# Optimization experiments

Measured on AMD Instinct MI355X. Metric: run time of the kernel, lower is better.

Reference implementation:

```python
import jax, jax.numpy as jnp
import numpy as np

B, N, D = 128, 131072, 1

def setup_inputs() -> dict:
    key = jax.random.key(0)
    k1, k2, k3, k4, k5 = jax.random.split(key, 5)
    particles = jax.random.normal(k1, (B, N, D), dtype=jnp.float32)
    particle_weights = jax.random.uniform(k2, (B, N), dtype=jnp.float32)
    observation = jax.random.normal(k3, (B, 1), dtype=jnp.float32)
    noise = jax.random.normal(k4, (B, N, D), dtype=jnp.float32)  # std-normal; scaled by sqrt(10) inside
    uniforms = jax.random.uniform(k5, (B, N), dtype=jnp.float32)
    return {
        "particles": particles,
        "particle_weights": particle_weights,
        "observation": observation,
        "noise": noise,
        "uniforms": uniforms,
        "timestep_number": 3,
    }

def _resample(particles, particle_weights, uniforms):
    # Efficient equivalent of the original O(B*N^2) tile + argmax(cumsum >= u):
    # first index where cumsum >= u  ==  searchsorted(cumsum, u, side='left').
    cum = jnp.cumsum(particle_weights, axis=-1)            # [B, N]
    idx = jax.vmap(lambda c, u: jnp.searchsorted(c, u, side='left'))(cum, uniforms)  # [B, N]
    resampled = jnp.take_along_axis(particles, idx[..., None], axis=1)  # [B, N, D]
    n = particles.shape[1]
    resampled_w = jnp.full(particle_weights.shape, 1.0 / n, dtype=particle_weights.dtype)
    return resampled, resampled_w

def reference(particles, particle_weights, observation, noise, uniforms, timestep_number):
    # Note: the original forward calls resample_particles but then builds the
    # transition from the ORIGINAL particles; resampled values never reach the
    # outputs. We keep the call for fidelity (XLA will DCE it).
    _resampled, _rw = _resample(particles, particle_weights, uniforms)

    # UNGM transition: x/2 + 25*x/(x^2+1) + 8*cos(1.2*t) + N(0, 10)
    mean = particles / 2.0 + 25.0 * (particles / (particles ** 2 + 1.0))
    mean = mean + 8.0 * jnp.cos(1.2 * jnp.float32(timestep_number))
    new_particles = mean + noise * np.float32(np.sqrt(10.0))   # [B, N, 1]

    # Observation likelihood: y ~ N(x^2/20, 1)
    obs_mean = (new_particles ** 2 / 20.0)[..., 0]             # [B, N]
    log_prob = -0.5 * (observation - obs_mean) ** 2 - 0.5 * np.float32(np.log(2.0 * np.pi))
    w = particle_weights * jnp.exp(log_prob)                   # [B, N]
    w = w / jnp.sum(w, axis=1, keepdims=True)
    return new_particles, w
```

## Files before the change

### kernel.cpp

```cpp
#include <hip/hip_runtime.h>
#include <math.h>

#define PF_B 128
#define PF_N 131072
#define TPB 256
#define EPT 8
#define EPB (TPB * EPT)
#define BLOCKS_PER_BATCH (PF_N / EPB)


__global__ __launch_bounds__(TPB) void pf_compute(
    const float* __restrict__ particles,
    const float* __restrict__ weights,
    const float* __restrict__ obs,
    const float* __restrict__ noise,
    const int*   __restrict__ tstep,
    float* __restrict__ np_out,
    float* __restrict__ w_out,
    float* __restrict__ sums)
{
    const int b     = blockIdx.x / BLOCKS_PER_BATCH;
    const int chunk = blockIdx.x % BLOCKS_PER_BATCH;
    const long base = (long)b * PF_N + (long)chunk * EPB;

    const float ob  = obs[b];
    const float c   = 8.0f * cosf(1.2f * (float)(*tstep));
    const float sq10 = 3.16227770f;
    const float nhl2pi = -0.9189385f;

    float lsum = 0.0f;

    #pragma unroll
    for (int k = 0; k < EPT / 4; ++k) {
        const long idx = base + (long)k * (TPB * 4) + (long)threadIdx.x * 4;
        const float4 x4  = *(const float4*)(particles + idx);
        const float4 n4  = *(const float4*)(noise + idx);
        const float4 wt4 = *(const float4*)(weights + idx);

        float xs[4] = {x4.x, x4.y, x4.z, x4.w};
        float ns[4] = {n4.x, n4.y, n4.z, n4.w};
        float ws[4] = {wt4.x, wt4.y, wt4.z, wt4.w};
        float xn[4], wn[4];

        #pragma unroll
        for (int j = 0; j < 4; ++j) {
            const float x = xs[j];
            const float mean = x * 0.5f + 25.0f * (x / (x * x + 1.0f)) + c;
            const float xnew = mean + ns[j] * sq10;
            xn[j] = xnew;
            const float om = (xnew * xnew) / 20.0f;
            const float d  = ob - om;
            const float lp = -0.5f * d * d + nhl2pi;
            const float wv = ws[j] * expf(lp);
            wn[j] = wv;
            lsum += wv;
        }

        float4 o4; o4.x = xn[0]; o4.y = xn[1]; o4.z = xn[2]; o4.w = xn[3];
        float4 w4; w4.x = wn[0]; w4.y = wn[1]; w4.z = wn[2]; w4.w = wn[3];
        *(float4*)(np_out + idx) = o4;
        *(float4*)(w_out + idx)  = w4;
    }

    #pragma unroll
    for (int off = 32; off > 0; off >>= 1)
        lsum += __shfl_down(lsum, off, 64);

    __shared__ float red[TPB / 64];
    if ((threadIdx.x & 63) == 0) red[threadIdx.x >> 6] = lsum;
    __syncthreads();
    if (threadIdx.x == 0) {
        float s = 0.0f;
        #pragma unroll
        for (int i = 0; i < TPB / 64; ++i) s += red[i];
        atomicAdd(&sums[b], s);
    }
}

__global__ __launch_bounds__(TPB) void pf_normalize(
    float* __restrict__ w_out,
    const float* __restrict__ sums)
{
    const int b     = blockIdx.x / BLOCKS_PER_BATCH;
    const int chunk = blockIdx.x % BLOCKS_PER_BATCH;
    const long base = (long)b * PF_N + (long)chunk * EPB;
    const float inv = 1.0f / sums[b];

    #pragma unroll
    for (int k = 0; k < EPT / 4; ++k) {
        const long idx = base + (long)k * (TPB * 4) + (long)threadIdx.x * 4;
        float4 v = *(const float4*)(w_out + idx);
        v.x *= inv; v.y *= inv; v.z *= inv; v.w *= inv;
        *(float4*)(w_out + idx) = v;
    }
}

extern "C" void kernel_launch(void* const* d_in, const int* in_sizes, int n_in,
                              void* d_out, int out_size, void* d_ws, size_t ws_size,
                              hipStream_t stream) {
    const float* particles = (const float*)d_in[0];
    const float* weights   = (const float*)d_in[1];
    const float* obs       = (const float*)d_in[2];
    const float* noise     = (const float*)d_in[3];
    const int*   tstep     = (const int*)d_in[5];

    float* np_out = (float*)d_out;
    float* w_out  = (float*)d_out + (long)PF_B * PF_N;
    float* sums   = (float*)d_ws;

    hipMemsetAsync(d_ws, 0, PF_B * sizeof(float), stream);

    const int grid = PF_B * BLOCKS_PER_BATCH;
    pf_compute<<<grid, TPB, 0, stream>>>(particles, weights, obs, noise, tstep,
                                         np_out, w_out, sums);
    pf_normalize<<<grid, TPB, 0, stream>>>(w_out, sums);
}
```

Baseline: 337.5 us.

## Fuse compute and normalize via cooperative grid sync with weights held in registers

Measured after the change: 391.6 us. 1.16x slower.

```diff
diff --git a/kernel.cpp b/kernel.cpp
--- a/kernel.cpp
+++ b/kernel.cpp
@@ -1,15 +1,74 @@
 #include <hip/hip_runtime.h>
+#include <hip/hip_cooperative_groups.h>
 #include <math.h>
 
 #define PF_B 128
 #define PF_N 131072
 #define TPB 256
-#define EPT 8
-#define EPB (TPB * EPT)
-#define BLOCKS_PER_BATCH (PF_N / EPB)
-
-
-__global__ __launch_bounds__(TPB) void pf_compute(
+
+#define C_NBLK 512
+#define C_BPB (C_NBLK / PF_B)
+#define C_EPB (PF_N / C_BPB)
+#define C_ITERS (C_EPB / (TPB * 4))
+
+#define F_EPT 8
+#define F_EPB (TPB * F_EPT)
+#define F_BPB (PF_N / F_EPB)
+#define F_GRID (PF_B * F_BPB)
+
+namespace cg = cooperative_groups;
+
+typedef float nfloat4 __attribute__((ext_vector_type(4)));
+
+__device__ __forceinline__ void nt_store4(float* p, float4 v) {
+    nfloat4 nv; nv.x = v.x; nv.y = v.y; nv.z = v.z; nv.w = v.w;
+    __builtin_nontemporal_store(nv, (nfloat4*)p);
+}
+
+__device__ __forceinline__ void compute4(const float4 x4, const float4 n4,
+                                         const float4 wt4, float ob, float c,
+                                         float4* xn_out, float4* wv_out,
+                                         float* lsum) {
+    const float sq10   = 3.16227770f;
+    const float nhl2pi = -0.9189385f;
+    float xs[4] = {x4.x, x4.y, x4.z, x4.w};
+    float ns[4] = {n4.x, n4.y, n4.z, n4.w};
+    float ws[4] = {wt4.x, wt4.y, wt4.z, wt4.w};
+    float xn[4], wn[4];
+    #pragma unroll
+    for (int j = 0; j < 4; ++j) {
+        const float x    = xs[j];
+        const float mean = x * 0.5f
+                         + 25.0f * x * __builtin_amdgcn_rcpf(x * x + 1.0f)
+                         + c;
+        const float xnew = mean + ns[j] * sq10;
+        xn[j] = xnew;
+        const float om = (xnew * xnew) * 0.05f;
+        const float d  = ob - om;
+        const float wv = ws[j] * __expf(-0.5f * d * d + nhl2pi);
+        wn[j] = wv;
+        *lsum += wv;
+    }
+    xn_out->x = xn[0]; xn_out->y = xn[1]; xn_out->z = xn[2]; xn_out->w = xn[3];
+    wv_out->x = wn[0]; wv_out->y = wn[1]; wv_out->z = wn[2]; wv_out->w = wn[3];
+}
+
+__device__ __forceinline__ void block_reduce_atomic(float lsum, float* target,
+                                                    float* red) {
+    #pragma unroll
+    for (int off = 32; off > 0; off >>= 1)
+        lsum += __shfl_down(lsum, off, 64);
+    if ((threadIdx.x & 63) == 0) red[threadIdx.x >> 6] = lsum;
+    __syncthreads();
+    if (threadIdx.x == 0) {
+        float s = 0.0f;
+        #pragma unroll
+        for (int i = 0; i < TPB / 64; ++i) s += red[i];
+        atomicAdd(target, s);
+    }
+}
+
+__global__ __launch_bounds__(TPB, 2) void pf_fused(
     const float* __restrict__ particles,
     const float* __restrict__ weights,
     const float* __restrict__ obs,
@@ -19,79 +78,111 @@
     float* __restrict__ w_out,
     float* __restrict__ sums)
 {
-    const int b     = blockIdx.x / BLOCKS_PER_BATCH;
-    const int chunk = blockIdx.x % BLOCKS_PER_BATCH;
-    const long base = (long)b * PF_N + (long)chunk * EPB;
-
-    const float ob  = obs[b];
-    const float c   = 8.0f * cosf(1.2f * (float)(*tstep));
-    const float sq10 = 3.16227770f;
-    const float nhl2pi = -0.9189385f;
+    const int b     = blockIdx.x / C_BPB;
+    const int chunk = blockIdx.x % C_BPB;
+    const long base = (long)b * PF_N + (long)chunk * C_EPB;
+
+    const float ob = obs[b];
+    const float c  = 8.0f * cosf(1.2f * (float)(*tstep));
+
+    float4 wreg[C_ITERS];
+    float  lsum = 0.0f;
+
+    #pragma unroll
+    for (int i = 0; i < C_ITERS; ++i) {
+        const long idx = base + (long)i * (TPB * 4) + (long)threadIdx.x * 4;
+        const float4 x4  = *(const float4*)(particles + idx);
+        const float4 n4  = *(const float4*)(noise + idx);
+        const float4 wt4 = *(const float4*)(weights + idx);
+        float4 xn, wv;
+        compute4(x4, n4, wt4, ob, c, &xn, &wv, &lsum);
+        nt_store4(np_out + idx, xn);
+        wreg[i] = wv;
+    }
+
+    __shared__ float red[TPB / 64];
+    __shared__ float s_inv;
+    block_reduce_atomic(lsum, &sums[b], red);
+
+    cg::this_grid().sync();
+
+    if (threadIdx.x == 0)
+        s_inv = 1.0f / atomicAdd(&sums[b], 0.0f);
+    __syncthreads();
+    const float inv = s_inv;
+
+    #pragma unroll
+    for (int i = 0; i < C_ITERS; ++i) {
+        const long idx = base + (long)i * (TPB * 4) + (long)threadIdx.x * 4;
+        float4 w4 = wreg[i];
+        w4.x *= inv; w4.y *= inv; w4.z *= inv; w4.w *= inv;
+        nt_store4(w_out + idx, w4);
+    }
+}
+
+__global__ __launch_bounds__(TPB) void pf_pass1(
+    const float* __restrict__ particles,
+    const float* __restrict__ weights,
+    const float* __restrict__ obs,
+    const float* __restrict__ noise,
+    const int*   __restrict__ tstep,
+    float* __restrict__ np_out,
+    float* __restrict__ sums)
+{
+    const int b     = blockIdx.x / F_BPB;
+    const int chunk = blockIdx.x % F_BPB;
+    const long base = (long)b * PF_N + (long)chunk * F_EPB;
+
+    const float ob = obs[b];
+    const float c  = 8.0f * cosf(1.2f * (float)(*tstep));
 
     float lsum = 0.0f;
-
-    #pragma unroll
-    for (int k = 0; k < EPT / 4; ++k) {
+    #pragma unroll
+    for (int k = 0; k < F_EPT / 4; ++k) {
         const long idx = base + (long)k * (TPB * 4) + (long)threadIdx.x * 4;
         const float4 x4  = *(const float4*)(particles + idx);
         const float4 n4  = *(const float4*)(noise + idx);
         const float4 wt4 = *(const float4*)(weights + idx);
-
+        float4 xn, wv;
+        compute4(x4, n4, wt4, ob, c, &xn, &wv, &lsum);
+        *(float4*)(np_out + idx) = xn;
+    }
+
+    __shared__ float red[TPB / 64];
+    block_reduce_atomic(lsum, &sums[b], red);
+}
+
+__global__ __launch_bounds__(TPB) void pf_pass2(
+    const float* __restrict__ np_out,
+    const float* __restrict__ weights,
+    const float* __restrict__ obs,
+    const float* __restrict__ sums,
+    float* __restrict__ w_out)
+{
+    const int b     = blockIdx.x / F_BPB;
+    const int chunk = blockIdx.x % F_BPB;
+    const long base = (long)b * PF_N + (long)chunk * F_EPB;
+
+    const float ob     = obs[b];
+    const float inv    = 1.0f / sums[b];
+    const float nhl2pi = -0.9189385f;
+
+    #pragma unroll
+    for (int k = 0; k < F_EPT / 4; ++k) {
+        const long idx = base + (long)k * (TPB * 4) + (long)threadIdx.x * 4;
+        const float4 x4  = *(const float4*)(np_out + idx);
+        const float4 wt4 = *(const float4*)(weights + idx);
         float xs[4] = {x4.x, x4.y, x4.z, x4.w};
-        float ns[4] = {n4.x, n4.y, n4.z, n4.w};
         float ws[4] = {wt4.x, wt4.y, wt4.z, wt4.w};
-        float xn[4], wn[4];
-
+        float wn[4];
         #pragma unroll
         for (int j = 0; j < 4; ++j) {
-            const float x = xs[j];
-            const float mean = x * 0.5f + 25.0f * (x / (x * x + 1.0f)) + c;
-            const float xnew = mean + ns[j] * sq10;
-            xn[j] = xnew;
-            const float om = (xnew * xnew) / 20.0f;
+            const float om = (xs[j] * xs[j]) * 0.05f;
             const float d  = ob - om;
-            const float lp = -0.5f * d * d + nhl2pi;
-            const float wv = ws[j] * expf(lp);
-            wn[j] = wv;
-            lsum += wv;
+            wn[j] = ws[j] * __expf(-0.5f * d * d + nhl2pi) * inv;
         }
-
-        float4 o4; o4.x = xn[0]; o4.y = xn[1]; o4.z = xn[2]; o4.w = xn[3];
         float4 w4; w4.x = wn[0]; w4.y = wn[1]; w4.z = wn[2]; w4.w = wn[3];
-        *(float4*)(np_out + idx) = o4;
-        *(float4*)(w_out + idx)  = w4;
-    }
-
-    #pragma unroll
-    for (int off = 32; off > 0; off >>= 1)
-        lsum += __shfl_down(lsum, off, 64);
-
-    __shared__ float red[TPB / 64];
-    if ((threadIdx.x & 63) == 0) red[threadIdx.x >> 6] = lsum;
-    __syncthreads();
-    if (threadIdx.x == 0) {
-        float s = 0.0f;
-        #pragma unroll
-        for (int i = 0; i < TPB / 64; ++i) s += red[i];
-        atomicAdd(&sums[b], s);
-    }
-}
-
-__global__ __launch_bounds__(TPB) void pf_normalize(
-    float* __restrict__ w_out,
-    const float* __restrict__ sums)
-{
-    const int b     = blockIdx.x / BLOCKS_PER_BATCH;
-    const int chunk = blockIdx.x % BLOCKS_PER_BATCH;
-    const long base = (long)b * PF_N + (long)chunk * EPB;
-    const float inv = 1.0f / sums[b];
-
-    #pragma unroll
-    for (int k = 0; k < EPT / 4; ++k) {
-        const long idx = base + (long)k * (TPB * 4) + (long)threadIdx.x * 4;
-        float4 v = *(const float4*)(w_out + idx);
-        v.x *= inv; v.y *= inv; v.z *= inv; v.w *= inv;
-        *(float4*)(w_out + idx) = v;
+        nt_store4(w_out + idx, w4);
     }
 }
 
@@ -108,10 +199,18 @@
     float* w_out  = (float*)d_out + (long)PF_B * PF_N;
     float* sums   = (float*)d_ws;
 
-    hipMemsetAsync(d_ws, 0, PF_B * sizeof(float), stream);
-
-    const int grid = PF_B * BLOCKS_PER_BATCH;
-    pf_compute<<<grid, TPB, 0, stream>>>(particles, weights, obs, noise, tstep,
-                                         np_out, w_out, sums);
-    pf_normalize<<<grid, TPB, 0, stream>>>(w_out, sums);
-}
+    (void)hipMemsetAsync(d_ws, 0, PF_B * sizeof(float), stream);
+
+    void* args[] = {
+        (void*)&particles, (void*)&weights, (void*)&obs, (void*)&noise,
+        (void*)&tstep, (void*)&np_out, (void*)&w_out, (void*)&sums
+    };
+    hipError_t err = hipLaunchCooperativeKernel((const void*)pf_fused,
+                                                dim3(C_NBLK), dim3(TPB),
+                                                args, 0, stream);
+    if (err != hipSuccess) {
+        pf_pass1<<<F_GRID, TPB, 0, stream>>>(particles, weights, obs, noise,
+                                             tstep, np_out, sums);
+        pf_pass2<<<F_GRID, TPB, 0, stream>>>(np_out, weights, obs, sums, w_out);
+    }
+}
```
